# Kernel tuning notes

Hardware: AMD Instinct MI355X
Metric: run time of the kernel (lower is better)

The kernel has to match this reference:

```python
import jax, jax.numpy as jnp
import numpy as np

K = 5
TAU = 0.5
N = 8192
IN_DIM = 128
OUT_DIM = 128


def setup_inputs() -> dict:
    key = jax.random.key(0)
    k1, k2, k3 = jax.random.split(key, 3)
    x = jax.random.normal(k1, (N, IN_DIM), dtype=jnp.float32)
    laplacian = jax.random.normal(k2, (N, N), dtype=jnp.float32) / np.sqrt(N)
    # xavier-uniform-like init for theta (K, in_dim, out_dim)
    limit = np.sqrt(6.0 / (IN_DIM + OUT_DIM))
    theta = jax.random.uniform(k3, (K, IN_DIM, OUT_DIM), dtype=jnp.float32,
                               minval=-limit, maxval=limit)
    return {"x": x, "laplacian": laplacian, "theta": theta}


def _cheb_coeff(k_order: int, tau: float) -> jnp.ndarray:
    # c_k = (2/K) * exp(-tau * cos(pi*(k+0.5)/K)), Chebyshev-Gauss nodes
    ks = jnp.arange(k_order, dtype=jnp.float32)
    x_k = jnp.cos(jnp.pi * (ks + 0.5) / k_order)
    return (2.0 / k_order) * jnp.exp(-tau * x_k)


def reference(x, laplacian, theta):
    coeff = _cheb_coeff(K, TAU)  # (K,)
    # Chebyshev recurrence: T_0 = x, T_1 = L x, T_k = 2 L T_{k-1} - T_{k-2}
    tx_prev, tx_curr = x, laplacian @ x
    tx_list = [tx_prev, tx_curr]
    for _ in range(2, K):
        tx_next = 2.0 * (laplacian @ tx_curr) - tx_prev
        tx_list.append(tx_next)
        tx_prev, tx_curr = tx_curr, tx_next
    tx_stack = jnp.stack(tx_list, axis=0)  # (K, N, in_dim)
    return jnp.einsum('kni,kio,k->no', tx_stack, theta, coeff)
```

## Files before the change

kernel.cpp:

```cpp
#include <hip/hip_runtime.h>
#include <hip/hip_bf16.h>
#include <cmath>

#define NROWS 8192
#define DIM   128
#define KDIM  8192
#define BM    64
#define BN    128
#define BK    64
#define SPLITK 4
#define KCHUNK (KDIM / SPLITK)
#define GITERS (KCHUNK / BK)
#define LDSTRIDE 80

typedef __bf16 bf16_t;
typedef __bf16 bf16x8 __attribute__((ext_vector_type(8)));
typedef __bf16 bf16x4 __attribute__((ext_vector_type(4)));
typedef float  f32x4  __attribute__((ext_vector_type(4)));

__global__ void k_cvt(const float* __restrict__ src, bf16_t* __restrict__ dst) {
    size_t i = ((size_t)blockIdx.x * 256 + threadIdx.x) * 8;
    float4 a = *(const float4*)(src + i);
    float4 b = *(const float4*)(src + i + 4);
    bf16x8 v;
    v[0] = (bf16_t)a.x; v[1] = (bf16_t)a.y; v[2] = (bf16_t)a.z; v[3] = (bf16_t)a.w;
    v[4] = (bf16_t)b.x; v[5] = (bf16_t)b.y; v[6] = (bf16_t)b.z; v[7] = (bf16_t)b.w;
    *(bf16x8*)(dst + i) = v;
}

__global__ void k_theta(const float* __restrict__ th, bf16_t* __restrict__ out,
                        float c0, float c1, float c2, float c3, float c4) {
    int idx = blockIdx.x * 256 + threadIdx.x;
    int k = idx >> 14;
    int o = (idx >> 7) & 127;
    int i = idx & 127;
    float c = (k == 0) ? c0 : (k == 1) ? c1 : (k == 2) ? c2 : (k == 3) ? c3 : c4;
    out[idx] = (bf16_t)(c * th[(k << 14) + (i << 7) + o]);
}

template <int MODE>
__global__ __launch_bounds__(256, 2)
void k_gemm(const void* __restrict__ Ap, const bf16_t* __restrict__ B,
            float* __restrict__ partial, bf16_t* __restrict__ Lbf_out) {
    __shared__ __align__(16) bf16_t As[BM * LDSTRIDE];
    __shared__ __align__(16) bf16_t Bs[BN * LDSTRIDE];

    const int t      = threadIdx.x;
    const int mTile  = blockIdx.x & 127;
    const int s      = blockIdx.x >> 7;
    const int mb     = mTile * BM;
    const int k0base = s * KCHUNK;
    const int wave = t >> 6, lane = t & 63;
    const int wM = (wave & 1) * 32;
    const int wN = (wave >> 1) * 64;
    const int lm = lane & 15, lk = lane >> 4;

    const int arow = t >> 3;
    const int asc  = t & 7;
    const int bkl  = t & 63;
    const int bn8  = t >> 6;

    f32x4 acc[2][4];
#pragma unroll
    for (int a = 0; a < 2; ++a)
#pragma unroll
        for (int b = 0; b < 4; ++b) acc[a][b] = (f32x4)0.0f;

    bf16x8 aR[2];
    float4 aRf[2][2];
    bf16x8 bR[4];

    auto loadT = [&](int kk) {
        const int k0 = k0base + kk * BK;
#pragma unroll
        for (int rep = 0; rep < 2; ++rep) {
            const int r = rep * 32 + arow;
            if (MODE == 0) {
                aR[rep] = *(const bf16x8*)((const bf16_t*)Ap +
                            (size_t)(mb + r) * KDIM + k0 + asc * 8);
            } else {
                const float* base = (const float*)Ap +
                            (size_t)(mb + r) * KDIM + k0 + asc * 8;
                aRf[rep][0] = *(const float4*)base;
                aRf[rep][1] = *(const float4*)(base + 4);
            }
        }
#pragma unroll
        for (int rep = 0; rep < 4; ++rep) {
            const int n8 = rep * 4 + bn8;
            bR[rep] = *(const bf16x8*)(B + (size_t)(k0 + bkl) * DIM + n8 * 8);
        }
    };

    auto storeT = [&](int kk) {
        const int k0 = k0base + kk * BK;
#pragma unroll
        for (int rep = 0; rep < 2; ++rep) {
            const int r = rep * 32 + arow;
            bf16x8 v;
            if (MODE == 0) {
                v = aR[rep];
            } else {
                v[0] = (bf16_t)aRf[rep][0].x; v[1] = (bf16_t)aRf[rep][0].y;
                v[2] = (bf16_t)aRf[rep][0].z; v[3] = (bf16_t)aRf[rep][0].w;
                v[4] = (bf16_t)aRf[rep][1].x; v[5] = (bf16_t)aRf[rep][1].y;
                v[6] = (bf16_t)aRf[rep][1].z; v[7] = (bf16_t)aRf[rep][1].w;
                if (MODE == 2)
                    *(bf16x8*)(Lbf_out + (size_t)(mb + r) * KDIM + k0 + asc * 8) = v;
            }
            *(bf16x8*)(&As[r * LDSTRIDE + asc * 8]) = v;
        }
#pragma unroll
        for (int rep = 0; rep < 4; ++rep) {
            const int n8 = rep * 4 + bn8;
            bf16x8 v = bR[rep];
#pragma unroll
            for (int q = 0; q < 8; ++q)
                Bs[(n8 * 8 + q) * LDSTRIDE + bkl] = v[q];
        }
    };

    loadT(0);
    for (int kk = 0; kk < GITERS; ++kk) {
        __syncthreads();
        storeT(kk);
        __syncthreads();
        if (kk + 1 < GITERS) loadT(kk + 1);
#pragma unroll
        for (int ko = 0; ko < 2; ++ko) {
            bf16x8 af[2], bfr[4];
#pragma unroll
            for (int tm = 0; tm < 2; ++tm)
                af[tm] = *(const bf16x8*)(&As[(wM + tm * 16 + lm) * LDSTRIDE +
                                              (ko * 4 + lk) * 8]);
#pragma unroll
            for (int tn = 0; tn < 4; ++tn)
                bfr[tn] = *(const bf16x8*)(&Bs[(wN + tn * 16 + lm) * LDSTRIDE +
                                               (ko * 4 + lk) * 8]);
#pragma unroll
            for (int tm = 0; tm < 2; ++tm)
#pragma unroll
                for (int tn = 0; tn < 4; ++tn)
                    acc[tm][tn] = __builtin_amdgcn_mfma_f32_16x16x32_bf16(
                        af[tm], bfr[tn], acc[tm][tn], 0, 0, 0);
        }
    }

    float* pOut = partial + (size_t)s * NROWS * DIM;
#pragma unroll
    for (int tm = 0; tm < 2; ++tm)
#pragma unroll
        for (int tn = 0; tn < 4; ++tn)
#pragma unroll
            for (int r = 0; r < 4; ++r) {
                const int row = mb + wM + tm * 16 + lk * 4 + r;
                const int col = wN + tn * 16 + lm;
                pOut[(size_t)row * DIM + col] = acc[tm][tn][r];
            }
}

__global__ void k_combine(const float* __restrict__ p, const float* __restrict__ prev,
                          float* __restrict__ f32dst, bf16_t* __restrict__ bfdst,
                          int first) {
    const size_t S = (size_t)NROWS * DIM;
    size_t i = ((size_t)blockIdx.x * 256 + threadIdx.x) * 4;
    float4 a = *(const float4*)(p + i);
    float4 b = *(const float4*)(p + S + i);
    float4 c = *(const float4*)(p + 2 * S + i);
    float4 d = *(const float4*)(p + 3 * S + i);
    float4 y;
    y.x = a.x + b.x + c.x + d.x;
    y.y = a.y + b.y + c.y + d.y;
    y.z = a.z + b.z + c.z + d.z;
    y.w = a.w + b.w + c.w + d.w;
    if (!first) {
        float4 pv = *(const float4*)(prev + i);
        y.x = 2.0f * y.x - pv.x;
        y.y = 2.0f * y.y - pv.y;
        y.z = 2.0f * y.z - pv.z;
        y.w = 2.0f * y.w - pv.w;
    }
    if (f32dst) *(float4*)(f32dst + i) = y;
    bf16x4 o;
    o[0] = (bf16_t)y.x; o[1] = (bf16_t)y.y; o[2] = (bf16_t)y.z; o[3] = (bf16_t)y.w;
    *(bf16x4*)(bfdst + i) = o;
}

__global__ __launch_bounds__(256, 2)
void k_proj(const bf16_t* __restrict__ T, const bf16_t* __restrict__ W,
            float* __restrict__ out) {
    __shared__ __align__(16) bf16_t As[BM * LDSTRIDE];
    __shared__ __align__(16) bf16_t Bs[BN * LDSTRIDE];

    const int t  = threadIdx.x;
    const int mb = blockIdx.x * BM;
    const int wave = t >> 6, lane = t & 63;
    const int wM = (wave & 1) * 32;
    const int wN = (wave >> 1) * 64;
    const int lm = lane & 15, lk = lane >> 4;
    const int arow = t >> 3;
    const int asc  = t & 7;
    const size_t S = (size_t)NROWS * DIM;

    f32x4 acc[2][4];
#pragma unroll
    for (int a = 0; a < 2; ++a)
#pragma unroll
        for (int b = 0; b < 4; ++b) acc[a][b] = (f32x4)0.0f;

    bf16x8 aR[2], bR[4];

    auto loadT = [&](int it) {
        const int seg = it >> 1;
        const int h   = (it & 1) * 64;
#pragma unroll
        for (int rep = 0; rep < 2; ++rep) {
            const int r = rep * 32 + arow;
            aR[rep] = *(const bf16x8*)(T + (size_t)seg * S +
                        (size_t)(mb + r) * DIM + h + asc * 8);
        }
#pragma unroll
        for (int rep = 0; rep < 4; ++rep) {
            const int o = rep * 32 + arow;
            bR[rep] = *(const bf16x8*)(W + seg * 16384 + o * 128 + h + asc * 8);
        }
    };
    auto storeT = [&]() {
#pragma unroll
        for (int rep = 0; rep < 2; ++rep) {
            const int r = rep * 32 + arow;
            *(bf16x8*)(&As[r * LDSTRIDE + asc * 8]) = aR[rep];
        }
#pragma unroll
        for (int rep = 0; rep < 4; ++rep) {
            const int o = rep * 32 + arow;
            *(bf16x8*)(&Bs[o * LDSTRIDE + asc * 8]) = bR[rep];
        }
    };

    loadT(0);
    for (int it = 0; it < 10; ++it) {
        __syncthreads();
        storeT();
        __syncthreads();
        if (it + 1 < 10) loadT(it + 1);
#pragma unroll
        for (int ko = 0; ko < 2; ++ko) {
            bf16x8 af[2], bfr[4];
#pragma unroll
            for (int tm = 0; tm < 2; ++tm)
                af[tm] = *(const bf16x8*)(&As[(wM + tm * 16 + lm) * LDSTRIDE +
                                              (ko * 4 + lk) * 8]);
#pragma unroll
            for (int tn = 0; tn < 4; ++tn)
                bfr[tn] = *(const bf16x8*)(&Bs[(wN + tn * 16 + lm) * LDSTRIDE +
                                               (ko * 4 + lk) * 8]);
#pragma unroll
            for (int tm = 0; tm < 2; ++tm)
#pragma unroll
                for (int tn = 0; tn < 4; ++tn)
                    acc[tm][tn] = __builtin_amdgcn_mfma_f32_16x16x32_bf16(
                        af[tm], bfr[tn], acc[tm][tn], 0, 0, 0);
        }
    }
#pragma unroll
    for (int tm = 0; tm < 2; ++tm)
#pragma unroll
        for (int tn = 0; tn < 4; ++tn)
#pragma unroll
            for (int r = 0; r < 4; ++r) {
                const int row = mb + wM + tm * 16 + lk * 4 + r;
                const int col = wN + tn * 16 + lm;
                out[(size_t)row * DIM + col] = acc[tm][tn][r];
            }
}

extern "C" void kernel_launch(void* const* d_in, const int* in_sizes, int n_in,
                              void* d_out, int out_size, void* d_ws, size_t ws_size,
                              hipStream_t stream) {
    const float* x  = nullptr;
    const float* L  = nullptr;
    const float* th = nullptr;
    for (int i = 0; i < n_in; ++i) {
        if (in_sizes[i] == NROWS * KDIM)      L  = (const float*)d_in[i];
        else if (in_sizes[i] == NROWS * DIM)  x  = (const float*)d_in[i];
        else if (in_sizes[i] == 5 * DIM * DIM) th = (const float*)d_in[i];
    }
    float* out = (float*)d_out;

    const size_t S = (size_t)NROWS * DIM;
    char* ws = (char*)d_ws;
    size_t off = 0;
    auto alloc = [&](size_t bytes) {
        void* p = ws + off;
        off = (off + bytes + 255) & ~(size_t)255;
        return p;
    };
    bf16_t* Tbf     = (bf16_t*)alloc(5 * S * 2);
    float*  Tf32    = (float*)alloc(2 * S * 4);
    bf16_t* thT     = (bf16_t*)alloc(5 * 128 * 128 * 2);
    float*  partial = (float*)alloc(SPLITK * S * 4);
    const size_t baseNeed = off;
    bf16_t* Lbf = (bf16_t*)(ws + off);
    const bool useLbf = (off + (size_t)NROWS * KDIM * 2) <= ws_size;
    if (baseNeed > ws_size) return;

    float c[5];
    for (int k = 0; k < 5; ++k)
        c[k] = (float)((2.0 / 5.0) * exp(-0.5 * cos(M_PI * (k + 0.5) / 5.0)));

    dim3 blk(256);
    k_cvt<<<512, blk, 0, stream>>>(x, Tbf);
    k_theta<<<320, blk, 0, stream>>>(th, thT, c[0], c[1], c[2], c[3], c[4]);

    for (int j = 1; j <= 4; ++j) {
        const bf16_t* Bj = Tbf + (size_t)(j - 1) * S;
        if (useLbf) {
            if (j == 1)
                k_gemm<2><<<512, blk, 0, stream>>>(L, Bj, partial, Lbf);
            else
                k_gemm<0><<<512, blk, 0, stream>>>(Lbf, Bj, partial, nullptr);
        } else {
            k_gemm<1><<<512, blk, 0, stream>>>(L, Bj, partial, nullptr);
        }
        const float* prev = nullptr;
        float* fdst = nullptr;
        if (j == 1)      { fdst = Tf32 + S; }
        else if (j == 2) { prev = x;        fdst = Tf32; }
        else if (j == 3) { prev = Tf32 + S; fdst = Tf32 + S; }
        else             { prev = Tf32;     fdst = nullptr; }
        k_combine<<<1024, blk, 0, stream>>>(partial, prev, fdst,
                                            Tbf + (size_t)j * S, j == 1 ? 1 : 0);
    }
    k_proj<<<128, blk, 0, stream>>>(Tbf, thT, out);
}
```

Before: 605.7 us.

## Double-buffer GEMM with async global-to-LDS loads and transposed B operand

Rewrites the Laplacian GEMM to stream bf16 tiles straight into double-buffered, XOR-swizzled LDS via global_load_lds. This removes the register-staged stores and one barrier per iteration. The combine kernel now also writes a transposed bf16 copy of each T_k, so B tiles load contiguously along K instead of being scattered element by element into LDS. L is converted to bf16 by a separate upfront kernel rather than inside the first GEMM, split-K doubles to 8, and occupancy hint rises to 3. The costs are more partial-sum traffic, an extra full pass over L, and no fallback when the workspace is too small.

Result: no change. 604.1 us (-0.3%).

```diff
diff --git a/kernel.cpp b/kernel.cpp
--- a/kernel.cpp
+++ b/kernel.cpp
@@ -8,7 +8,7 @@
 #define BM    64
 #define BN    128
 #define BK    64
-#define SPLITK 4
+#define SPLITK 8
 #define KCHUNK (KDIM / SPLITK)
 #define GITERS (KCHUNK / BK)
 #define LDSTRIDE 80
@@ -18,7 +18,13 @@
 typedef __bf16 bf16x4 __attribute__((ext_vector_type(4)));
 typedef float  f32x4  __attribute__((ext_vector_type(4)));
 
-__global__ void k_cvt(const float* __restrict__ src, bf16_t* __restrict__ dst) {
+__device__ __forceinline__ void async16(const void* g, void* l) {
+    __builtin_amdgcn_global_load_lds(
+        (const __attribute__((address_space(1))) unsigned int*)g,
+        (__attribute__((address_space(3))) unsigned int*)l, 16, 0, 0);
+}
+
+__global__ void k_cvtL(const float* __restrict__ src, bf16_t* __restrict__ dst) {
     size_t i = ((size_t)blockIdx.x * 256 + threadIdx.x) * 8;
     float4 a = *(const float4*)(src + i);
     float4 b = *(const float4*)(src + i + 4);
@@ -38,27 +44,23 @@
     out[idx] = (bf16_t)(c * th[(k << 14) + (i << 7) + o]);
 }
 
-template <int MODE>
-__global__ __launch_bounds__(256, 2)
-void k_gemm(const void* __restrict__ Ap, const bf16_t* __restrict__ B,
-            float* __restrict__ partial, bf16_t* __restrict__ Lbf_out) {
-    __shared__ __align__(16) bf16_t As[BM * LDSTRIDE];
-    __shared__ __align__(16) bf16_t Bs[BN * LDSTRIDE];
-
-    const int t      = threadIdx.x;
-    const int mTile  = blockIdx.x & 127;
-    const int s      = blockIdx.x >> 7;
-    const int mb     = mTile * BM;
+__global__ __launch_bounds__(256, 3)
+void k_gemm(const bf16_t* __restrict__ A, const bf16_t* __restrict__ Bt,
+            float* __restrict__ partial) {
+    __shared__ __align__(16) bf16_t As[2][BM * BK];
+    __shared__ __align__(16) bf16_t Bs[2][BN * BK];
+
+    const int t     = threadIdx.x;
+    const int mTile = blockIdx.x & 127;
+    const int s     = blockIdx.x >> 7;
+    const int mb    = mTile * BM;
     const int k0base = s * KCHUNK;
     const int wave = t >> 6, lane = t & 63;
     const int wM = (wave & 1) * 32;
     const int wN = (wave >> 1) * 64;
     const int lm = lane & 15, lk = lane >> 4;
-
-    const int arow = t >> 3;
-    const int asc  = t & 7;
-    const int bkl  = t & 63;
-    const int bn8  = t >> 6;
+    const int lrow = lane >> 3;
+    const int lsrc = (lane & 7) ^ lrow;
 
     f32x4 acc[2][4];
 #pragma unroll
@@ -66,77 +68,41 @@
 #pragma unroll
         for (int b = 0; b < 4; ++b) acc[a][b] = (f32x4)0.0f;
 
-    bf16x8 aR[2];
-    float4 aRf[2][2];
-    bf16x8 bR[4];
-
-    auto loadT = [&](int kk) {
+    auto stage = [&](int kk, int buf) {
         const int k0 = k0base + kk * BK;
 #pragma unroll
-        for (int rep = 0; rep < 2; ++rep) {
-            const int r = rep * 32 + arow;
-            if (MODE == 0) {
-                aR[rep] = *(const bf16x8*)((const bf16_t*)Ap +
-                            (size_t)(mb + r) * KDIM + k0 + asc * 8);
-            } else {
-                const float* base = (const float*)Ap +
-                            (size_t)(mb + r) * KDIM + k0 + asc * 8;
-                aRf[rep][0] = *(const float4*)base;
-                aRf[rep][1] = *(const float4*)(base + 4);
-            }
-        }
-#pragma unroll
-        for (int rep = 0; rep < 4; ++rep) {
-            const int n8 = rep * 4 + bn8;
-            bR[rep] = *(const bf16x8*)(B + (size_t)(k0 + bkl) * DIM + n8 * 8);
+        for (int i = 0; i < 2; ++i) {
+            const int r = wave * 16 + i * 8 + lrow;
+            async16(A + (size_t)(mb + r) * KDIM + k0 + lsrc * 8,
+                    &As[buf][(wave * 16 + i * 8) * BK]);
+        }
+#pragma unroll
+        for (int i = 0; i < 4; ++i) {
+            const int n = wave * 32 + i * 8 + lrow;
+            async16(Bt + (size_t)n * KDIM + k0 + lsrc * 8,
+                    &Bs[buf][(wave * 32 + i * 8) * BK]);
         }
     };
 
-    auto storeT = [&](int kk) {
-        const int k0 = k0base + kk * BK;
-#pragma unroll
-        for (int rep = 0; rep < 2; ++rep) {
-            const int r = rep * 32 + arow;
-            bf16x8 v;
-            if (MODE == 0) {
-                v = aR[rep];
-            } else {
-                v[0] = (bf16_t)aRf[rep][0].x; v[1] = (bf16_t)aRf[rep][0].y;
-                v[2] = (bf16_t)aRf[rep][0].z; v[3] = (bf16_t)aRf[rep][0].w;
-                v[4] = (bf16_t)aRf[rep][1].x; v[5] = (bf16_t)aRf[rep][1].y;
-                v[6] = (bf16_t)aRf[rep][1].z; v[7] = (bf16_t)aRf[rep][1].w;
-                if (MODE == 2)
-                    *(bf16x8*)(Lbf_out + (size_t)(mb + r) * KDIM + k0 + asc * 8) = v;
-            }
-            *(bf16x8*)(&As[r * LDSTRIDE + asc * 8]) = v;
-        }
-#pragma unroll
-        for (int rep = 0; rep < 4; ++rep) {
-            const int n8 = rep * 4 + bn8;
-            bf16x8 v = bR[rep];
-#pragma unroll
-            for (int q = 0; q < 8; ++q)
-                Bs[(n8 * 8 + q) * LDSTRIDE + bkl] = v[q];
-        }
-    };
-
-    loadT(0);
+    stage(0, 0);
+    __syncthreads();
     for (int kk = 0; kk < GITERS; ++kk) {
-        __syncthreads();
-        storeT(kk);
-        __syncthreads();
-        if (kk + 1 < GITERS) loadT(kk + 1);
+        const int buf = kk & 1;
+        if (kk + 1 < GITERS) stage(kk + 1, buf ^ 1);
 #pragma unroll
         for (int ko = 0; ko < 2; ++ko) {
             bf16x8 af[2], bfr[4];
-#pragma unroll
-            for (int tm = 0; tm < 2; ++tm)
-                af[tm] = *(const bf16x8*)(&As[(wM + tm * 16 + lm) * LDSTRIDE +
-                                              (ko * 4 + lk) * 8]);
-#pragma unroll
-            for (int tn = 0; tn < 4; ++tn)
-                bfr[tn] = *(const bf16x8*)(&Bs[(wN + tn * 16 + lm) * LDSTRIDE +
-                                               (ko * 4 + lk) * 8]);
+            const int csX = (ko * 4 + lk) ^ (lm & 7);
+#pragma unroll
+            for (int tm = 0; tm < 2; ++tm) {
+                const int r = wM + tm * 16 + lm;
+                af[tm] = *(const bf16x8*)(&As[buf][r * BK + csX * 8]);
+            }
+#pragma unroll
+            for (int tn = 0; tn < 4; ++tn) {
+                const int n = wN + tn * 16 + lm;
+                bfr[tn] = *(const bf16x8*)(&Bs[buf][n * BK + csX * 8]);
+            }
 #pragma unroll
             for (int tm = 0; tm < 2; ++tm)
 #pragma unroll
@@ -144,6 +110,7 @@
                     acc[tm][tn] = __builtin_amdgcn_mfma_f32_16x16x32_bf16(
                         af[tm], bfr[tn], acc[tm][tn], 0, 0, 0);
         }
+        __syncthreads();
     }
 
     float* pOut = partial + (size_t)s * NROWS * DIM;
@@ -159,31 +126,63 @@
             }
 }
 
-__global__ void k_combine(const float* __restrict__ p, const float* __restrict__ prev,
-                          float* __restrict__ f32dst, bf16_t* __restrict__ bfdst,
-                          int first) {
+template <int MODE>
+__global__ void k_combine(const float* __restrict__ src, const float* __restrict__ prev,
+                          float* __restrict__ f32dst, bf16_t* __restrict__ tbf,
+                          bf16_t* __restrict__ bt) {
+    __shared__ bf16_t tl[128 * 24];
     const size_t S = (size_t)NROWS * DIM;
-    size_t i = ((size_t)blockIdx.x * 256 + threadIdx.x) * 4;
-    float4 a = *(const float4*)(p + i);
-    float4 b = *(const float4*)(p + S + i);
-    float4 c = *(const float4*)(p + 2 * S + i);
-    float4 d = *(const float4*)(p + 3 * S + i);
-    float4 y;
-    y.x = a.x + b.x + c.x + d.x;
-    y.y = a.y + b.y + c.y + d.y;
-    y.z = a.z + b.z + c.z + d.z;
-    y.w = a.w + b.w + c.w + d.w;
-    if (!first) {
-        float4 pv = *(const float4*)(prev + i);
-        y.x = 2.0f * y.x - pv.x;
-        y.y = 2.0f * y.y - pv.y;
-        y.z = 2.0f * y.z - pv.z;
-        y.w = 2.0f * y.w - pv.w;
-    }
-    if (f32dst) *(float4*)(f32dst + i) = y;
-    bf16x4 o;
-    o[0] = (bf16_t)y.x; o[1] = (bf16_t)y.y; o[2] = (bf16_t)y.z; o[3] = (bf16_t)y.w;
-    *(bf16x4*)(bfdst + i) = o;
+    const int t  = threadIdx.x;
+    const int n0 = blockIdx.x * 16;
+    const int nl = t >> 4;
+    const int dp = (t & 15) * 8;
+    const int n  = n0 + nl;
+
+    float y[8];
+    if (MODE == 0) {
+        float4 a = *(const float4*)(src + (size_t)n * DIM + dp);
+        float4 b = *(const float4*)(src + (size_t)n * DIM + dp + 4);
+        y[0] = a.x; y[1] = a.y; y[2] = a.z; y[3] = a.w;
+        y[4] = b.x; y[5] = b.y; y[6] = b.z; y[7] = b.w;
+    } else {
+#pragma unroll
+        for (int j = 0; j < 8; ++j) y[j] = 0.0f;
+#pragma unroll
+        for (int ss = 0; ss < SPLITK; ++ss) {
+            const float* p = src + (size_t)ss * S + (size_t)n * DIM + dp;
+            float4 a = *(const float4*)p;
+            float4 b = *(const float4*)(p + 4);
+            y[0] += a.x; y[1] += a.y; y[2] += a.z; y[3] += a.w;
+            y[4] += b.x; y[5] += b.y; y[6] += b.z; y[7] += b.w;
+        }
+        if (MODE == 2) {
+            float4 a = *(const float4*)(prev + (size_t)n * DIM + dp);
+            float4 b = *(const float4*)(prev + (size_t)n * DIM + dp + 4);
+            y[0] = 2.0f * y[0] - a.x; y[1] = 2.0f * y[1] - a.y;
+            y[2] = 2.0f * y[2] - a.z; y[3] = 2.0f * y[3] - a.w;
+            y[4] = 2.0f * y[4] - b.x; y[5] = 2.0f * y[5] - b.y;
+            y[6] = 2.0f * y[6] - b.z; y[7] = 2.0f * y[7] - b.w;
+        }
+    }
+    if (f32dst) {
+        float4 a, b;
+        a.x = y[0]; a.y = y[1]; a.z = y[2]; a.w = y[3];
+        b.x = y[4]; b.y = y[5]; b.z = y[6]; b.w = y[7];
+        *(float4*)(f32dst + (size_t)n * DIM + dp) = a;
+        *(float4*)(f32dst + (size_t)n * DIM + dp + 4) = b;
+    }
+    bf16x8 v;
+#pragma unroll
+    for (int j = 0; j < 8; ++j) v[j] = (bf16_t)y[j];
+    *(bf16x8*)(tbf + (size_t)n * DIM + dp) = v;
+    if (bt) {
+#pragma unroll
+        for (int j = 0; j < 8; ++j) tl[(dp + j) * 24 + nl] = v[j];
+        __syncthreads();
+        const int d = t >> 1, h = (t & 1) * 8;
+        bf16x8 w = *(const bf16x8*)(&tl[d * 24 + h]);
+        *(bf16x8*)(bt + (size_t)d * NROWS + n0 + h) = w;
+    }
 }
 
 __global__ __launch_bounds__(256, 2)
@@ -282,8 +281,8 @@
     const float* L  = nullptr;
     const float* th = nullptr;
     for (int i = 0; i < n_in; ++i) {
-        if (in_sizes[i] == NROWS * KDIM)      L  = (const float*)d_in[i];
-        else if (in_sizes[i] == NROWS * DIM)  x  = (const float*)d_in[i];
+        if (in_sizes[i] == NROWS * KDIM)       L  = (const float*)d_in[i];
+        else if (in_sizes[i] == NROWS * DIM)   x  = (const float*)d_in[i];
         else if (in_sizes[i] == 5 * DIM * DIM) th = (const float*)d_in[i];
     }
     float* out = (float*)d_out;
@@ -297,40 +296,34 @@
         return p;
     };
     bf16_t* Tbf     = (bf16_t*)alloc(5 * S * 2);
+    bf16_t* Bt      = (bf16_t*)alloc(5 * S * 2);
     float*  Tf32    = (float*)alloc(2 * S * 4);
     bf16_t* thT     = (bf16_t*)alloc(5 * 128 * 128 * 2);
-    float*  partial = (float*)alloc(SPLITK * S * 4);
-    const size_t baseNeed = off;
-    bf16_t* Lbf = (bf16_t*)(ws + off);
-    const bool useLbf = (off + (size_t)NROWS * KDIM * 2) <= ws_size;
-    if (baseNeed > ws_size) return;
+    float*  partial = (float*)alloc((size_t)SPLITK * S * 4);
+    bf16_t* Lbf     = (bf16_t*)alloc((size_t)NROWS * KDIM * 2);
+    if (off > ws_size) return;
 
     float c[5];
     for (int k = 0; k < 5; ++k)
         c[k] = (float)((2.0 / 5.0) * exp(-0.5 * cos(M_PI * (k + 0.5) / 5.0)));
 
     dim3 blk(256);
-    k_cvt<<<512, blk, 0, stream>>>(x, Tbf);
+    k_cvtL<<<32768, blk, 0, stream>>>(L, Lbf);
+    k_combine<0><<<512, blk, 0, stream>>>(x, nullptr, nullptr, Tbf, Bt);
     k_theta<<<320, blk, 0, stream>>>(th, thT, c[0], c[1], c[2], c[3], c[4]);
 
     for (int j = 1; j <= 4; ++j) {
-        const bf16_t* Bj = Tbf + (size_t)(j - 1) * S;
-        if (useLbf) {
-            if (j == 1)
-                k_gemm<2><<<512, blk, 0, stream>>>(L, Bj, partial, Lbf);
-            else
-                k_gemm<0><<<512, blk, 0, stream>>>(Lbf, Bj, partial, nullptr);
-        } else {
-            k_gemm<1><<<512, blk, 0, stream>>>(L, Bj, partial, nullptr);
-        }
-        const float* prev = nullptr;
-        float* fdst = nullptr;
-        if (j == 1)      { fdst = Tf32 + S; }
-        else if (j == 2) { prev = x;        fdst = Tf32; }
-        else if (j == 3) { prev = Tf32 + S; fdst = Tf32 + S; }
-        else             { prev = Tf32;     fdst = nullptr; }
-        k_combine<<<1024, blk, 0, stream>>>(partial, prev, fdst,
-                                            Tbf + (size_t)j * S, j == 1 ? 1 : 0);
+        k_gemm<<<1024, blk, 0, stream>>>(Lbf, Bt + (size_t)(j - 1) * S, partial);
+        bf16_t* tbf = Tbf + (size_t)j * S;
+        bf16_t* bt  = (j < 4) ? Bt + (size_t)j * S : nullptr;
+        if (j == 1)
+            k_combine<1><<<512, blk, 0, stream>>>(partial, nullptr, Tf32 + S, tbf, bt);
+        else if (j == 2)
+            k_combine<2><<<512, blk, 0, stream>>>(partial, x, Tf32, tbf, bt);
+        else if (j == 3)
+            k_combine<2><<<512, blk, 0, stream>>>(partial, Tf32 + S, Tf32 + S, tbf, bt);
+        else
+            k_combine<2><<<512, blk, 0, stream>>>(partial, Tf32, nullptr, tbf, nullptr);
     }
     k_proj<<<128, blk, 0, stream>>>(Tbf, thT, out);
 }
```
